# Kernel tuning notes

Measured on AMD Instinct MI355X. Metric: run time of the kernel, lower is better.

The kernel has to match this reference:

```python
import jax, jax.numpy as jnp
import numpy as np

D_MODEL = 64


def setup_inputs() -> dict:
    key = jax.random.key(0)
    kq, kk, kv, km = jax.random.split(key, 4)
    B, S, d = 8, 4096, D_MODEL
    Q = jax.random.normal(kq, (B, S, d), dtype=jnp.float32)
    K = jax.random.normal(kk, (B, S, d), dtype=jnp.float32)
    V = jax.random.normal(kv, (B, S, d), dtype=jnp.float32)
    mask = jax.random.uniform(km, (S, S), dtype=jnp.float32)
    return {"Q": Q, "K": K, "V": V, "mask": mask}


def reference(Q, K, V, mask):
    scale = 1.0 / np.sqrt(D_MODEL).astype(np.float32)
    # scores: [B, S, S]
    scores = jnp.einsum("bqd,bkd->bqk", Q, K) * scale
    probs = jax.nn.softmax(scores, axis=-1)
    # post-softmax multiplicative mask + renormalization over masked probs
    masked = probs * mask[None, :, :]
    masked = masked / jnp.sum(masked, axis=-1, keepdims=True)
    return jnp.einsum("bqk,bkd->bqd", masked, V)
```

## Files before the change

### kernel.cpp

```cpp
#include <hip/hip_runtime.h>
#include <hip/hip_bf16.h>

#define S_LEN 4096
#define DMODEL 64
#define QBLK 128
#define NQT (S_LEN / QBLK)
#define KBLK 32
#define NKT (S_LEN / KBLK)
#define NSPLIT 4
#define NROWS ((size_t)8 * S_LEN)
#define NELEM ((size_t)8 * S_LEN * DMODEL)
#define TSZ 2048
#define MH 2048
#define QSCALE 0.180336880f

typedef __attribute__((ext_vector_type(8))) short bf16x8;
typedef __attribute__((ext_vector_type(4))) float f32x4;
typedef __attribute__((ext_vector_type(8))) unsigned short us8;
typedef __attribute__((ext_vector_type(4))) unsigned int u32x4;

#define LDS_BARRIER()                                            \
    do {                                                         \
        asm volatile("s_waitcnt lgkmcnt(0)" ::: "memory");       \
        __builtin_amdgcn_s_barrier();                            \
    } while (0)

__device__ __forceinline__ unsigned short f2bf(float f) {
    unsigned int u = __builtin_bit_cast(unsigned int, f);
    u += 0x7FFFu + ((u >> 16) & 1u);
    return (unsigned short)(u >> 16);
}
__device__ __forceinline__ unsigned int packbf2(float lo, float hi) {
    __hip_bfloat162 h = __float22bfloat162_rn(float2{lo, hi});
    unsigned int w;
    __builtin_memcpy(&w, &h, sizeof(w));
    return w;
}
__device__ __forceinline__ float ub(unsigned int w, int i) {
    return (float)((w >> (8 * i)) & 0xFFu);
}
__device__ __forceinline__ bf16x8 cvt8s(const float* __restrict__ p, float c) {
    f32x4 a = *(const f32x4*)p;
    f32x4 b = *(const f32x4*)(p + 4);
    bf16x8 r;
    r[0] = (short)f2bf(a[0] * c); r[1] = (short)f2bf(a[1] * c);
    r[2] = (short)f2bf(a[2] * c); r[3] = (short)f2bf(a[3] * c);
    r[4] = (short)f2bf(b[0] * c); r[5] = (short)f2bf(b[1] * c);
    r[6] = (short)f2bf(b[2] * c); r[7] = (short)f2bf(b[3] * c);
    return r;
}
__device__ __forceinline__ unsigned int q8(float m) {
    return (unsigned int)(m * 255.f + 0.5f);
}

__global__ __launch_bounds__(256)
void convert_all(const float* __restrict__ K, const float* __restrict__ V,
                 const float* __restrict__ M,
                 unsigned short* __restrict__ Ktt, unsigned short* __restrict__ Vtt,
                 unsigned char* __restrict__ Mu) {
    const int t = threadIdx.x;
    int bid = blockIdx.x;

    if (bid < 1024) {
        const int b  = bid >> 7;
        const int kt = bid & 127;
        const int l = t & 63, frag = t >> 6;
        const int j = l & 15, g = l >> 4;
        const int row = kt * KBLK + ((frag >> 1) & 1) * 16 + j;
        const int col = (frag & 1) * 32 + g * 8;
        const float* src = K + ((size_t)b * S_LEN + row) * DMODEL + col;
        f32x4 a = *(const f32x4*)src;
        f32x4 c = *(const f32x4*)(src + 4);
        us8 o;
        o[0] = f2bf(a[0]); o[1] = f2bf(a[1]); o[2] = f2bf(a[2]); o[3] = f2bf(a[3]);
        o[4] = f2bf(c[0]); o[5] = f2bf(c[1]); o[6] = f2bf(c[2]); o[7] = f2bf(c[3]);
        *(us8*)(Ktt + ((size_t)(b * NKT + kt)) * TSZ + t * 8) = o;
    } else if (bid < 2048) {
        bid -= 1024;
        __shared__ unsigned short lk[KBLK][68];
        const int b  = bid >> 7;
        const int kt = bid & 127;
        {
            const int key = t >> 3, d0 = (t & 7) * 8;
            const float* src = V + ((size_t)b * S_LEN + kt * KBLK + key) * DMODEL + d0;
            f32x4 a = *(const f32x4*)src;
            f32x4 c = *(const f32x4*)(src + 4);
            lk[key][d0 + 0] = f2bf(a[0]); lk[key][d0 + 1] = f2bf(a[1]);
            lk[key][d0 + 2] = f2bf(a[2]); lk[key][d0 + 3] = f2bf(a[3]);
            lk[key][d0 + 4] = f2bf(c[0]); lk[key][d0 + 5] = f2bf(c[1]);
            lk[key][d0 + 6] = f2bf(c[2]); lk[key][d0 + 7] = f2bf(c[3]);
        }
        __syncthreads();
        {
            const int l = t & 63, dt = t >> 6;
            const int j = l & 15, g = l >> 4;
            us8 o;
            #pragma unroll
            for (int e = 0; e < 8; ++e) {
                const int key = 16 * (e >> 2) + 4 * g + (e & 3);
                o[e] = lk[key][dt * 16 + j];
            }
            *(us8*)(Vtt + ((size_t)(b * NKT + kt)) * TSZ + t * 8) = o;
        }
    } else {
        bid -= 2048;
        const int qt  = bid >> 8;
        const int rem = bid & 255;
        const int kt  = rem >> 1;
        const int h   = rem & 1;
        const int l = t & 63, w = t >> 6;
        const int j = l & 15, g = l >> 4;
        const int row = qt * QBLK + w * 32 + h * 16 + j;
        const float* src = M + ((size_t)row) * S_LEN + kt * KBLK;
        f32x4 a = *(const f32x4*)(src + 4 * g);
        f32x4 c = *(const f32x4*)(src + 16 + 4 * g);
        uint2 o;
        o.x = q8(a[0]) | (q8(a[1]) << 8) | (q8(a[2]) << 16) | (q8(a[3]) << 24);
        o.y = q8(c[0]) | (q8(c[1]) << 8) | (q8(c[2]) << 16) | (q8(c[3]) << 24);
        *(uint2*)(Mu + (((size_t)(qt * NKT + kt)) * 2 + h) * MH + t * 8) = o;
    }
}

template <int SPLITS>
__global__ __launch_bounds__(256, 4)
void attn_frag(const float* __restrict__ Q,
               const unsigned short* __restrict__ Ktt,
               const unsigned short* __restrict__ Vtt,
               const unsigned char* __restrict__ Mu,
               float* __restrict__ Pacc, float* __restrict__ Plsum,
               float* __restrict__ O) {
    __shared__ __align__(16) unsigned short S[8192];

    const int t    = threadIdx.x;
    const int wave = t >> 6;
    const int l    = t & 63;
    const int g    = l >> 4;
    const int j    = l & 15;

    const int bid = blockIdx.x;
    const int b   = bid & 7;
    const int qt  = (bid >> 3) & 31;
    const int sp  = (SPLITS > 1) ? (bid >> 8) : 0;
    const int nsteps = NKT / SPLITS;
    const int qrowA = qt * QBLK + wave * 32 + j;
    const int qrowB = qrowA + 16;
    const size_t rowA = (size_t)b * S_LEN + qrowA;
    const size_t rowB = rowA + 16;

    const float* Qb = Q + (size_t)b * S_LEN * DMODEL;
    const bf16x8 qf0a = cvt8s(Qb + (size_t)qrowA * DMODEL + g * 8, QSCALE);
    const bf16x8 qf1a = cvt8s(Qb + (size_t)qrowA * DMODEL + g * 8 + 32, QSCALE);
    const bf16x8 qf0b = cvt8s(Qb + (size_t)qrowB * DMODEL + g * 8, QSCALE);
    const bf16x8 qf1b = cvt8s(Qb + (size_t)qrowB * DMODEL + g * 8 + 32, QSCALE);

    bf16x8 vones;
    #pragma unroll
    for (int e = 0; e < 8; ++e) vones[e] = (short)0x3F80;

    f32x4 accA[4], accB[4];
    #pragma unroll
    for (int dt = 0; dt < 4; ++dt) {
        accA[dt] = f32x4{0.f, 0.f, 0.f, 0.f};
        accB[dt] = f32x4{0.f, 0.f, 0.f, 0.f};
    }
    f32x4 acclA = {0.f, 0.f, 0.f, 0.f};
    f32x4 acclB = {0.f, 0.f, 0.f, 0.f};

    const int kt0 = sp * nsteps;
    const unsigned short* pk = Ktt + (size_t)(b * NKT + kt0) * TSZ + t * 8;
    const unsigned short* pv = Vtt + (size_t)(b * NKT + kt0) * TSZ + t * 8;
    const unsigned char*  pm = Mu + ((size_t)(qt * NKT + kt0) * 2) * MH + t * 8;

    us8 kreg = *(const us8*)pk;
    us8 vreg = *(const us8*)pv;
    uint2 mA0 = *(const uint2*)pm;
    uint2 mA1 = *(const uint2*)(pm + MH);
    *(us8*)&S[t * 8]        = kreg;
    *(us8*)&S[4096 + t * 8] = vreg;
    kreg = *(const us8*)(pk + TSZ);
    vreg = *(const us8*)(pv + TSZ);
    uint2 mB0 = *(const uint2*)(pm + 2 * MH);
    uint2 mB1 = *(const uint2*)(pm + 3 * MH);
    pk += 2 * TSZ; pv += 2 * TSZ; pm += 4 * MH;
    LDS_BARRIER();

    for (int p = 0; p < nsteps / 2; ++p) {
        #pragma unroll
        for (int u = 0; u < 2; ++u) {
            *(us8*)&S[(u ^ 1) * 2048 + t * 8]        = kreg;
            *(us8*)&S[4096 + (u ^ 1) * 2048 + t * 8] = vreg;

            kreg = *(const us8*)pk; pk += TSZ;
            vreg = *(const us8*)pv; pv += TSZ;

            bf16x8 kf0 = *(const bf16x8*)&S[u * 2048 + 0 * 512 + l * 8];
            bf16x8 kf1 = *(const bf16x8*)&S[u * 2048 + 1 * 512 + l * 8];
            bf16x8 kf2 = *(const bf16x8*)&S[u * 2048 + 2 * 512 + l * 8];
            bf16x8 kf3 = *(const bf16x8*)&S[u * 2048 + 3 * 512 + l * 8];

            f32x4 sA0 = {0.f, 0.f, 0.f, 0.f}, sA1 = {0.f, 0.f, 0.f, 0.f};
            f32x4 sB0 = {0.f, 0.f, 0.f, 0.f}, sB1 = {0.f, 0.f, 0.f, 0.f};
            sA0 = __builtin_amdgcn_mfma_f32_16x16x32_bf16(kf0, qf0a, sA0, 0, 0, 0);
            sB0 = __builtin_amdgcn_mfma_f32_16x16x32_bf16(kf0, qf0b, sB0, 0, 0, 0);
            sA0 = __builtin_amdgcn_mfma_f32_16x16x32_bf16(kf1, qf1a, sA0, 0, 0, 0);
            sB0 = __builtin_amdgcn_mfma_f32_16x16x32_bf16(kf1, qf1b, sB0, 0, 0, 0);
            sA1 = __builtin_amdgcn_mfma_f32_16x16x32_bf16(kf2, qf0a, sA1, 0, 0, 0);
            sB1 = __builtin_amdgcn_mfma_f32_16x16x32_bf16(kf2, qf0b, sB1, 0, 0, 0);
            sA1 = __builtin_amdgcn_mfma_f32_16x16x32_bf16(kf3, qf1a, sA1, 0, 0, 0);
            sB1 = __builtin_amdgcn_mfma_f32_16x16x32_bf16(kf3, qf1b, sB1, 0, 0, 0);

            const uint2 m0 = u ? mB0 : mA0;
            const uint2 m1 = u ? mB1 : mA1;

            float eA0[4], eA1[4], eB0[4], eB1[4];
            #pragma unroll
            for (int r = 0; r < 4; ++r) {
                eA0[r] = __builtin_amdgcn_exp2f(sA0[r]) * ub(m0.x, r);
                eA1[r] = __builtin_amdgcn_exp2f(sA1[r]) * ub(m0.y, r);
                eB0[r] = __builtin_amdgcn_exp2f(sB0[r]) * ub(m1.x, r);
                eB1[r] = __builtin_amdgcn_exp2f(sB1[r]) * ub(m1.y, r);
            }
            u32x4 pwA, pwB;
            pwA[0] = packbf2(eA0[0], eA0[1]); pwA[1] = packbf2(eA0[2], eA0[3]);
            pwA[2] = packbf2(eA1[0], eA1[1]); pwA[3] = packbf2(eA1[2], eA1[3]);
            pwB[0] = packbf2(eB0[0], eB0[1]); pwB[1] = packbf2(eB0[2], eB0[3]);
            pwB[2] = packbf2(eB1[0], eB1[1]); pwB[3] = packbf2(eB1[2], eB1[3]);
            const bf16x8 pfA = __builtin_bit_cast(bf16x8, pwA);
            const bf16x8 pfB = __builtin_bit_cast(bf16x8, pwB);

            if (u == 0) { mA0 = *(const uint2*)pm; mA1 = *(const uint2*)(pm + MH); }
            else        { mB0 = *(const uint2*)pm; mB1 = *(const uint2*)(pm + MH); }
            pm += 2 * MH;

            acclA = __builtin_amdgcn_mfma_f32_16x16x32_bf16(vones, pfA, acclA, 0, 0, 0);
            acclB = __builtin_amdgcn_mfma_f32_16x16x32_bf16(vones, pfB, acclB, 0, 0, 0);
            #pragma unroll
            for (int dt = 0; dt < 4; ++dt) {
                bf16x8 vf = *(const bf16x8*)&S[4096 + u * 2048 + dt * 512 + l * 8];
                accA[dt] = __builtin_amdgcn_mfma_f32_16x16x32_bf16(vf, pfA, accA[dt], 0, 0, 0);
                accB[dt] = __builtin_amdgcn_mfma_f32_16x16x32_bf16(vf, pfB, accB[dt], 0, 0, 0);
            }

            LDS_BARRIER();
        }
    }

    const float lsumA = acclA[0];
    const float lsumB = acclB[0];

    if (SPLITS > 1) {
        if (g == 0) {
            Plsum[(size_t)sp * NROWS + rowA] = lsumA;
            Plsum[(size_t)sp * NROWS + rowB] = lsumB;
        }
        float* prA = Pacc + ((size_t)sp * NROWS + rowA) * DMODEL;
        float* prB = Pacc + ((size_t)sp * NROWS + rowB) * DMODEL;
        #pragma unroll
        for (int dt = 0; dt < 4; ++dt) {
            *(f32x4*)(prA + dt * 16 + g * 4) = accA[dt];
            *(f32x4*)(prB + dt * 16 + g * 4) = accB[dt];
        }
    } else {
        const float invA = 1.0f / lsumA;
        const float invB = 1.0f / lsumB;
        float* orA = O + rowA * DMODEL;
        float* orB = O + rowB * DMODEL;
        #pragma unroll
        for (int dt = 0; dt < 4; ++dt) {
            f32x4 oa, ob;
            #pragma unroll
            for (int r = 0; r < 4; ++r) { oa[r] = accA[dt][r] * invA; ob[r] = accB[dt][r] * invB; }
            *(f32x4*)(orA + dt * 16 + g * 4) = oa;
            *(f32x4*)(orB + dt * 16 + g * 4) = ob;
        }
    }
}

template <int SPLITS>
__global__ __launch_bounds__(256)
void reduce_split(const float* __restrict__ Pacc, const float* __restrict__ Plsum,
                  float* __restrict__ O) {
    const int t = threadIdx.x;
    const size_t rid = (size_t)blockIdx.x * 16 + (t >> 4);
    const int seg = (t & 15) * 4;

    float ls = 0.f;
    f32x4 a = {0.f, 0.f, 0.f, 0.f};
    #pragma unroll
    for (int s = 0; s < SPLITS; ++s) {
        ls += Plsum[(size_t)s * NROWS + rid];
        f32x4 v = *(const f32x4*)(Pacc + ((size_t)s * NROWS + rid) * DMODEL + seg);
        a[0] += v[0]; a[1] += v[1]; a[2] += v[2]; a[3] += v[3];
    }
    const float inv = 1.0f / ls;
    f32x4 o = {a[0] * inv, a[1] * inv, a[2] * inv, a[3] * inv};
    *(f32x4*)(O + rid * DMODEL + seg) = o;
}

__global__ __launch_bounds__(256)
void attn_fb(const float* __restrict__ Q, const float* __restrict__ Kf,
             const float* __restrict__ Vf, const float* __restrict__ M,
             float* __restrict__ O) {
    const int t    = threadIdx.x;
    const int wave = t >> 6;
    const int lane = t & 63;
    const int g    = lane >> 4;
    const int j    = lane & 15;
    const int bid  = blockIdx.x;
    const int b    = bid & 7;
    const int qt   = bid >> 3;
    const int qrow = qt * 64 + wave * 16 + j;

    const float* Qb = Q + (size_t)b * S_LEN * DMODEL;
    const bf16x8 qf0 = cvt8s(Qb + (size_t)qrow * DMODEL + g * 8, QSCALE);
    const bf16x8 qf1 = cvt8s(Qb + (size_t)qrow * DMODEL + g * 8 + 32, QSCALE);

    f32x4 acc[4];
    #pragma unroll
    for (int dt = 0; dt < 4; ++dt) acc[dt] = f32x4{0.f, 0.f, 0.f, 0.f};
    float lsum = 0.f;

    const float* Kfb = Kf + (size_t)b * S_LEN * DMODEL;
    const float* Vfb = Vf + (size_t)b * S_LEN * DMODEL;
    const float* mrow = M + (size_t)qrow * S_LEN;

    int kg[8];
    #pragma unroll
    for (int e = 0; e < 8; ++e) kg[e] = 16 * (e >> 2) + 4 * g + (e & 3);

    for (int kt = 0; kt < NKT; ++kt) {
        const int kb = kt * KBLK;
        bf16x8 kf00 = cvt8s(Kfb + (size_t)(kb + j) * DMODEL + g * 8, 1.0f);
        bf16x8 kf01 = cvt8s(Kfb + (size_t)(kb + j) * DMODEL + g * 8 + 32, 1.0f);
        bf16x8 kf10 = cvt8s(Kfb + (size_t)(kb + 16 + j) * DMODEL + g * 8, 1.0f);
        bf16x8 kf11 = cvt8s(Kfb + (size_t)(kb + 16 + j) * DMODEL + g * 8 + 32, 1.0f);

        f32x4 st0 = {0.f, 0.f, 0.f, 0.f};
        f32x4 st1 = {0.f, 0.f, 0.f, 0.f};
        st0 = __builtin_amdgcn_mfma_f32_16x16x32_bf16(kf00, qf0, st0, 0, 0, 0);
        st0 = __builtin_amdgcn_mfma_f32_16x16x32_bf16(kf01, qf1, st0, 0, 0, 0);
        st1 = __builtin_amdgcn_mfma_f32_16x16x32_bf16(kf10, qf0, st1, 0, 0, 0);
        st1 = __builtin_amdgcn_mfma_f32_16x16x32_bf16(kf11, qf1, st1, 0, 0, 0);

        f32x4 m0 = *(const f32x4*)(mrow + kb + g * 4);
        f32x4 m1 = *(const f32x4*)(mrow + kb + 16 + g * 4);

        bf16x8 pf;
        #pragma unroll
        for (int r = 0; r < 4; ++r) {
            float w0 = __builtin_amdgcn_exp2f(st0[r]) * m0[r];
            float w1 = __builtin_amdgcn_exp2f(st1[r]) * m1[r];
            lsum += w0 + w1;
            pf[r]     = (short)f2bf(w0);
            pf[4 + r] = (short)f2bf(w1);
        }

        #pragma unroll
        for (int dt = 0; dt < 4; ++dt) {
            bf16x8 vf;
            #pragma unroll
            for (int e = 0; e < 8; ++e)
                vf[e] = (short)f2bf(Vfb[(size_t)(kb + kg[e]) * DMODEL + dt * 16 + j]);
            acc[dt] = __builtin_amdgcn_mfma_f32_16x16x32_bf16(vf, pf, acc[dt], 0, 0, 0);
        }
    }

    lsum += __shfl_xor(lsum, 16, 64);
    lsum += __shfl_xor(lsum, 32, 64);
    const float inv = 1.0f / lsum;

    float* orow = O + ((size_t)b * S_LEN + qrow) * DMODEL;
    #pragma unroll
    for (int dt = 0; dt < 4; ++dt) {
        f32x4 o;
        #pragma unroll
        for (int r = 0; r < 4; ++r) o[r] = acc[dt][r] * inv;
        *(f32x4*)(orow + dt * 16 + g * 4) = o;
    }
}

extern "C" void kernel_launch(void* const* d_in, const int* in_sizes, int n_in,
                              void* d_out, int out_size, void* d_ws, size_t ws_size,
                              hipStream_t stream) {
    const float* Q = (const float*)d_in[0];
    const float* K = (const float*)d_in[1];
    const float* V = (const float*)d_in[2];
    const float* M = (const float*)d_in[3];
    float* O = (float*)d_out;

    const size_t bytes_kv = 2 * NELEM * 2;
    const size_t bytes_mu = (size_t)S_LEN * S_LEN;

    unsigned short* Ktt = (unsigned short*)d_ws;
    unsigned short* Vtt = Ktt + NELEM;
    unsigned char*  Mu  = (unsigned char*)(Vtt + NELEM);

    const size_t need4 = bytes_kv + bytes_mu + (size_t)NSPLIT * NROWS * 4
                       + (size_t)NSPLIT * NROWS * DMODEL * 4;

    if (ws_size >= need4) {
        float* Plsum = (float*)((char*)d_ws + bytes_kv + bytes_mu);
        float* Pacc  = Plsum + (size_t)NSPLIT * NROWS;
        convert_all<<<10240, 256, 0, stream>>>(K, V, M, Ktt, Vtt, Mu);
        attn_frag<NSPLIT><<<8 * NQT * NSPLIT, 256, 0, stream>>>(
            Q, Ktt, Vtt, Mu, Pacc, Plsum, O);
        reduce_split<NSPLIT><<<(int)(NROWS / 16), 256, 0, stream>>>(Pacc, Plsum, O);
    } else {
        attn_fb<<<512, 256, 0, stream>>>(Q, K, V, M, O);
    }
}
```

Before: 86.62 us.

## Double query block to 256 rows so each wave processes 64 query rows

Raises the query tile per workgroup from 128 to 256 rows, so each wave handles four 16-row chunks instead of two. Every K/V tile staged in LDS is reused across twice as many queries, halving K/V traffic and barriers per query row. The mask pre-pack layout changes to match, and launch bounds drop to 2 blocks per SM to allow the larger accumulator register set. The cost is more registers, lower occupancy and half as many attention blocks, which may leave the GPU less full.

```diff
diff --git a/kernel.cpp b/kernel.cpp
--- a/kernel.cpp
+++ b/kernel.cpp
@@ -3,7 +3,7 @@
 
 #define S_LEN 4096
 #define DMODEL 64
-#define QBLK 128
+#define QBLK 256
 #define NQT (S_LEN / QBLK)
 #define KBLK 32
 #define NKT (S_LEN / KBLK)
@@ -104,25 +104,25 @@
         }
     } else {
         bid -= 2048;
-        const int qt  = bid >> 8;
-        const int rem = bid & 255;
-        const int kt  = rem >> 1;
-        const int h   = rem & 1;
+        const int qt  = bid >> 9;
+        const int rem = bid & 511;
+        const int kt  = rem >> 2;
+        const int h   = rem & 3;
         const int l = t & 63, w = t >> 6;
         const int j = l & 15, g = l >> 4;
-        const int row = qt * QBLK + w * 32 + h * 16 + j;
+        const int row = qt * QBLK + w * 64 + h * 16 + j;
         const float* src = M + ((size_t)row) * S_LEN + kt * KBLK;
         f32x4 a = *(const f32x4*)(src + 4 * g);
         f32x4 c = *(const f32x4*)(src + 16 + 4 * g);
         uint2 o;
         o.x = q8(a[0]) | (q8(a[1]) << 8) | (q8(a[2]) << 16) | (q8(a[3]) << 24);
         o.y = q8(c[0]) | (q8(c[1]) << 8) | (q8(c[2]) << 16) | (q8(c[3]) << 24);
-        *(uint2*)(Mu + (((size_t)(qt * NKT + kt)) * 2 + h) * MH + t * 8) = o;
+        *(uint2*)(Mu + (((size_t)(qt * NKT + kt)) * 4 + h) * MH + t * 8) = o;
     }
 }
 
 template <int SPLITS>
-__global__ __launch_bounds__(256, 4)
+__global__ __launch_bounds__(256, 2)
 void attn_frag(const float* __restrict__ Q,
                const unsigned short* __restrict__ Ktt,
                const unsigned short* __restrict__ Vtt,
@@ -139,49 +139,50 @@
 
     const int bid = blockIdx.x;
     const int b   = bid & 7;
-    const int qt  = (bid >> 3) & 31;
-    const int sp  = (SPLITS > 1) ? (bid >> 8) : 0;
+    const int qt  = (bid >> 3) & 15;
+    const int sp  = (SPLITS > 1) ? (bid >> 7) : 0;
     const int nsteps = NKT / SPLITS;
-    const int qrowA = qt * QBLK + wave * 32 + j;
-    const int qrowB = qrowA + 16;
-    const size_t rowA = (size_t)b * S_LEN + qrowA;
-    const size_t rowB = rowA + 16;
+    const int qrow0 = qt * QBLK + wave * 64 + j;
+    const size_t row0 = (size_t)b * S_LEN + qrow0;
 
     const float* Qb = Q + (size_t)b * S_LEN * DMODEL;
-    const bf16x8 qf0a = cvt8s(Qb + (size_t)qrowA * DMODEL + g * 8, QSCALE);
-    const bf16x8 qf1a = cvt8s(Qb + (size_t)qrowA * DMODEL + g * 8 + 32, QSCALE);
-    const bf16x8 qf0b = cvt8s(Qb + (size_t)qrowB * DMODEL + g * 8, QSCALE);
-    const bf16x8 qf1b = cvt8s(Qb + (size_t)qrowB * DMODEL + g * 8 + 32, QSCALE);
+    bf16x8 qf0[4], qf1[4];
+    #pragma unroll
+    for (int c = 0; c < 4; ++c) {
+        qf0[c] = cvt8s(Qb + (size_t)(qrow0 + 16 * c) * DMODEL + g * 8, QSCALE);
+        qf1[c] = cvt8s(Qb + (size_t)(qrow0 + 16 * c) * DMODEL + g * 8 + 32, QSCALE);
+    }
 
     bf16x8 vones;
     #pragma unroll
     for (int e = 0; e < 8; ++e) vones[e] = (short)0x3F80;
 
-    f32x4 accA[4], accB[4];
-    #pragma unroll
-    for (int dt = 0; dt < 4; ++dt) {
-        accA[dt] = f32x4{0.f, 0.f, 0.f, 0.f};
-        accB[dt] = f32x4{0.f, 0.f, 0.f, 0.f};
-    }
-    f32x4 acclA = {0.f, 0.f, 0.f, 0.f};
-    f32x4 acclB = {0.f, 0.f, 0.f, 0.f};
+    f32x4 acc[4][4];
+    f32x4 accl[4];
+    #pragma unroll
+    for (int c = 0; c < 4; ++c) {
+        accl[c] = f32x4{0.f, 0.f, 0.f, 0.f};
+        #pragma unroll
+        for (int dt = 0; dt < 4; ++dt) acc[c][dt] = f32x4{0.f, 0.f, 0.f, 0.f};
+    }
 
     const int kt0 = sp * nsteps;
     const unsigned short* pk = Ktt + (size_t)(b * NKT + kt0) * TSZ + t * 8;
     const unsigned short* pv = Vtt + (size_t)(b * NKT + kt0) * TSZ + t * 8;
-    const unsigned char*  pm = Mu + ((size_t)(qt * NKT + kt0) * 2) * MH + t * 8;
+    const unsigned char*  pm = Mu + ((size_t)(qt * NKT + kt0) * 4) * MH + t * 8;
 
     us8 kreg = *(const us8*)pk;
     us8 vreg = *(const us8*)pv;
-    uint2 mA0 = *(const uint2*)pm;
-    uint2 mA1 = *(const uint2*)(pm + MH);
+    uint2 mA[4], mB[4];
+    #pragma unroll
+    for (int c = 0; c < 4; ++c) mA[c] = *(const uint2*)(pm + c * MH);
     *(us8*)&S[t * 8]        = kreg;
     *(us8*)&S[4096 + t * 8] = vreg;
     kreg = *(const us8*)(pk + TSZ);
     vreg = *(const us8*)(pv + TSZ);
-    uint2 mB0 = *(const uint2*)(pm + 2 * MH);
-    uint2 mB1 = *(const uint2*)(pm + 3 * MH);
-    pk += 2 * TSZ; pv += 2 * TSZ; pm += 4 * MH;
+    #pragma unroll
+    for (int c = 0; c < 4; ++c) mB[c] = *(const uint2*)(pm + (4 + c) * MH);
+    pk += 2 * TSZ; pv += 2 * TSZ; pm += 8 * MH;
     LDS_BARRIER();
 
     for (int p = 0; p < nsteps / 2; ++p) {
@@ -198,80 +199,73 @@
             bf16x8 kf2 = *(const bf16x8*)&S[u * 2048 + 2 * 512 + l * 8];
             bf16x8 kf3 = *(const bf16x8*)&S[u * 2048 + 3 * 512 + l * 8];
 
-            f32x4 sA0 = {0.f, 0.f, 0.f, 0.f}, sA1 = {0.f, 0.f, 0.f, 0.f};
-            f32x4 sB0 = {0.f, 0.f, 0.f, 0.f}, sB1 = {0.f, 0.f, 0.f, 0.f};
-            sA0 = __builtin_amdgcn_mfma_f32_16x16x32_bf16(kf0, qf0a, sA0, 0, 0, 0);
-            sB0 = __builtin_amdgcn_mfma_f32_16x16x32_bf16(kf0, qf0b, sB0, 0, 0, 0);
-            sA0 = __builtin_amdgcn_mfma_f32_16x16x32_bf16(kf1, qf1a, sA0, 0, 0, 0);
-            sB0 = __builtin_amdgcn_mfma_f32_16x16x32_bf16(kf1, qf1b, sB0, 0, 0, 0);
-            sA1 = __builtin_amdgcn_mfma_f32_16x16x32_bf16(kf2, qf0a, sA1, 0, 0, 0);
-            sB1 = __builtin_amdgcn_mfma_f32_16x16x32_bf16(kf2, qf0b, sB1, 0, 0, 0);
-            sA1 = __builtin_amdgcn_mfma_f32_16x16x32_bf16(kf3, qf1a, sA1, 0, 0, 0);
-            sB1 = __builtin_amdgcn_mfma_f32_16x16x32_bf16(kf3, qf1b, sB1, 0, 0, 0);
-
-            const uint2 m0 = u ? mB0 : mA0;
-            const uint2 m1 = u ? mB1 : mA1;
-
-            float eA0[4], eA1[4], eB0[4], eB1[4];
-            #pragma unroll
-            for (int r = 0; r < 4; ++r) {
-                eA0[r] = __builtin_amdgcn_exp2f(sA0[r]) * ub(m0.x, r);
-                eA1[r] = __builtin_amdgcn_exp2f(sA1[r]) * ub(m0.y, r);
-                eB0[r] = __builtin_amdgcn_exp2f(sB0[r]) * ub(m1.x, r);
-                eB1[r] = __builtin_amdgcn_exp2f(sB1[r]) * ub(m1.y, r);
+            bf16x8 pf[4];
+            #pragma unroll
+            for (int c = 0; c < 4; ++c) {
+                f32x4 s0 = {0.f, 0.f, 0.f, 0.f}, s1 = {0.f, 0.f, 0.f, 0.f};
+                s0 = __builtin_amdgcn_mfma_f32_16x16x32_bf16(kf0, qf0[c], s0, 0, 0, 0);
+                s0 = __builtin_amdgcn_mfma_f32_16x16x32_bf16(kf1, qf1[c], s0, 0, 0, 0);
+                s1 = __builtin_amdgcn_mfma_f32_16x16x32_bf16(kf2, qf0[c], s1, 0, 0, 0);
+                s1 = __builtin_amdgcn_mfma_f32_16x16x32_bf16(kf3, qf1[c], s1, 0, 0, 0);
+
+                const uint2 m = u ? mB[c] : mA[c];
+                float e0[4], e1[4];
+                #pragma unroll
+                for (int r = 0; r < 4; ++r) {
+                    e0[r] = __builtin_amdgcn_exp2f(s0[r]) * ub(m.x, r);
+                    e1[r] = __builtin_amdgcn_exp2f(s1[r]) * ub(m.y, r);
+                }
+                u32x4 pw;
+                pw[0] = packbf2(e0[0], e0[1]); pw[1] = packbf2(e0[2], e0[3]);
+                pw[2] = packbf2(e1[0], e1[1]); pw[3] = packbf2(e1[2], e1[3]);
+                pf[c] = __builtin_bit_cast(bf16x8, pw);
+
+                accl[c] = __builtin_amdgcn_mfma_f32_16x16x32_bf16(vones, pf[c], accl[c], 0, 0, 0);
             }
-            u32x4 pwA, pwB;
-            pwA[0] = packbf2(eA0[0], eA0[1]); pwA[1] = packbf2(eA0[2], eA0[3]);
-            pwA[2] = packbf2(eA1[0], eA1[1]); pwA[3] = packbf2(eA1[2], eA1[3]);
-            pwB[0] = packbf2(eB0[0], eB0[1]); pwB[1] = packbf2(eB0[2], eB0[3]);
-            pwB[2] = packbf2(eB1[0], eB1[1]); pwB[3] = packbf2(eB1[2], eB1[3]);
-            const bf16x8 pfA = __builtin_bit_cast(bf16x8, pwA);
-            const bf16x8 pfB = __builtin_bit_cast(bf16x8, pwB);
-
-            if (u == 0) { mA0 = *(const uint2*)pm; mA1 = *(const uint2*)(pm + MH); }
-            else        { mB0 = *(const uint2*)pm; mB1 = *(const uint2*)(pm + MH); }
-            pm += 2 * MH;
-
-            acclA = __builtin_amdgcn_mfma_f32_16x16x32_bf16(vones, pfA, acclA, 0, 0, 0);
-            acclB = __builtin_amdgcn_mfma_f32_16x16x32_bf16(vones, pfB, acclB, 0, 0, 0);
+
+            if (u == 0) {
+                #pragma unroll
+                for (int c = 0; c < 4; ++c) mA[c] = *(const uint2*)(pm + c * MH);
+            } else {
+                #pragma unroll
+                for (int c = 0; c < 4; ++c) mB[c] = *(const uint2*)(pm + c * MH);
+            }
+            pm += 4 * MH;
+
             #pragma unroll
             for (int dt = 0; dt < 4; ++dt) {
                 bf16x8 vf = *(const bf16x8*)&S[4096 + u * 2048 + dt * 512 + l * 8];
-                accA[dt] = __builtin_amdgcn_mfma_f32_16x16x32_bf16(vf, pfA, accA[dt], 0, 0, 0);
-                accB[dt] = __builtin_amdgcn_mfma_f32_16x16x32_bf16(vf, pfB, accB[dt], 0, 0, 0);
+                #pragma unroll
+                for (int c = 0; c < 4; ++c)
+                    acc[c][dt] = __builtin_amdgcn_mfma_f32_16x16x32_bf16(vf, pf[c], acc[c][dt], 0, 0, 0);
             }
 
             LDS_BARRIER();
         }
     }
 
-    const float lsumA = acclA[0];
-    const float lsumB = acclB[0];
-
     if (SPLITS > 1) {
-        if (g == 0) {
-            Plsum[(size_t)sp * NROWS + rowA] = lsumA;
-            Plsum[(size_t)sp * NROWS + rowB] = lsumB;
-        }
-        float* prA = Pacc + ((size_t)sp * NROWS + rowA) * DMODEL;
-        float* prB = Pacc + ((size_t)sp * NROWS + rowB) * DMODEL;
-        #pragma unroll
-        for (int dt = 0; dt < 4; ++dt) {
-            *(f32x4*)(prA + dt * 16 + g * 4) = accA[dt];
-            *(f32x4*)(prB + dt * 16 + g * 4) = accB[dt];
+        #pragma unroll
+        for (int c = 0; c < 4; ++c) {
+            const size_t row = row0 + 16 * c;
+            if (g == 0) Plsum[(size_t)sp * NROWS + row] = accl[c][0];
+            float* pr = Pacc + ((size_t)sp * NROWS + row) * DMODEL;
+            #pragma unroll
+            for (int dt = 0; dt < 4; ++dt)
+                *(f32x4*)(pr + dt * 16 + g * 4) = acc[c][dt];
         }
     } else {
-        const float invA = 1.0f / lsumA;
-        const float invB = 1.0f / lsumB;
-        float* orA = O + rowA * DMODEL;
-        float* orB = O + rowB * DMODEL;
-        #pragma unroll
-        for (int dt = 0; dt < 4; ++dt) {
-            f32x4 oa, ob;
-            #pragma unroll
-            for (int r = 0; r < 4; ++r) { oa[r] = accA[dt][r] * invA; ob[r] = accB[dt][r] * invB; }
-            *(f32x4*)(orA + dt * 16 + g * 4) = oa;
-            *(f32x4*)(orB + dt * 16 + g * 4) = ob;
+        #pragma unroll
+        for (int c = 0; c < 4; ++c) {
+            const float inv = 1.0f / accl[c][0];
+            float* orow = O + (row0 + 16 * c) * DMODEL;
+            #pragma unroll
+            for (int dt = 0; dt < 4; ++dt) {
+                f32x4 o;
+                #pragma unroll
+                for (int r = 0; r < 4; ++r) o[r] = acc[c][dt][r] * inv;
+                *(f32x4*)(orow + dt * 16 + g * 4) = o;
+            }
         }
     }
 }
```

Result: faster. 84.86 us (-2.0%).
